# Performance work log

Hardware: AMD Instinct MI355X
Metric: run time of the kernel (lower is better)

Reference implementation:

```python
import jax, jax.numpy as jnp
import numpy as np

W0, W1 = 14, 14            # window size
NUM_HEADS = 12
DIM = 768
HEAD_DIM = DIM // NUM_HEADS
N_TOK = W0 * W1 + 1        # 197 (with cls token)
BATCH = 64


def _mask_1d_rel_pos_index(s):
    i = np.arange(s)
    return i[None, :] - i[:, None] + s - 1


def _add_cls(index, num_tokens, offset):
    index = index.reshape(num_tokens, num_tokens)
    new = np.zeros((num_tokens + 1, num_tokens + 1), dtype=np.int32)
    new[1:, 1:] = index
    new[0, :] = offset
    new[:, 0] = offset + 1
    new[0, 0] = offset + 2
    return new


def _build_rel_indices():
    nt = W0 * W1
    h = _mask_1d_rel_pos_index(W0).reshape(W0, 1, W0, 1)
    h = np.broadcast_to(h, (W0, W1, W0, W1))
    h_index = _add_cls(h, nt, 2 * W0 - 1)
    w = _mask_1d_rel_pos_index(W1).reshape(1, W1, 1, W1)
    w = np.broadcast_to(w, (W0, W1, W0, W1))
    w_index = _add_cls(w, nt, 2 * W1 - 1)
    return jnp.asarray(h_index), jnp.asarray(w_index)


def setup_inputs() -> dict:
    key = jax.random.key(0)
    ks = jax.random.split(key, 6)
    h_index, w_index = _build_rel_indices()
    return {
        "x": jax.random.normal(ks[0], (BATCH, N_TOK, DIM), dtype=jnp.float32),
        "qkv_w": jax.random.normal(ks[1], (3 * DIM, DIM), dtype=jnp.float32) * 0.02,
        "q_bias": jnp.zeros((DIM,), dtype=jnp.float32),
        "v_bias": jnp.zeros((DIM,), dtype=jnp.float32),
        "proj_w": jax.random.normal(ks[2], (DIM, DIM), dtype=jnp.float32) * 0.02,
        "proj_b": jnp.zeros((DIM,), dtype=jnp.float32),
        "rpb_high": jax.random.normal(ks[3], (2 * W0 + 2, NUM_HEADS), dtype=jnp.float32) * 0.02,
        "rpb_width": jax.random.normal(ks[4], (2 * W1 + 2, NUM_HEADS), dtype=jnp.float32) * 0.02,
        "h_index": h_index,
        "w_index": w_index,
    }


def reference(x, qkv_w, q_bias, v_bias, proj_w, proj_b, rpb_high, rpb_width,
              h_index, w_index):
    B, N, C = x.shape
    scale = HEAD_DIM ** (-0.5)
    # fused qkv with (q_bias, 0, v_bias) bias as in torch source
    bias = jnp.concatenate([q_bias, jnp.zeros_like(v_bias), v_bias])
    qkv = x @ qkv_w.T + bias                             # [B, N, 3*C]
    qkv = qkv.reshape(B, N, 3, NUM_HEADS, HEAD_DIM).transpose(2, 0, 3, 1, 4)
    q, k, v = qkv[0], qkv[1], qkv[2]                     # [B, H, N, hd]
    q = q * scale
    # qk_float=True -> scores in float32
    attn = jnp.einsum('bhnd,bhmd->bhnm',
                      q.astype(jnp.float32), k.astype(jnp.float32))
    # decoupled relative position bias: two embedding lookups, summed
    rpb = rpb_high[h_index] + rpb_width[w_index]         # [N, N, H]
    rpb = rpb.transpose(2, 0, 1)                         # [H, N, N]
    attn = attn + rpb[None].astype(attn.dtype)
    attn = jax.nn.softmax(attn, axis=-1).astype(x.dtype)
    out = jnp.einsum('bhnm,bhmd->bnhd', attn, v).reshape(B, N, C)
    return out @ proj_w.T + proj_b
```

## Files before the change

### kernel.cpp

```cpp
#include <hip/hip_runtime.h>
#include <hip/hip_bf16.h>
#include <cstdint>
#include <cstddef>

using fx4  = __attribute__((ext_vector_type(4))) float;
using bfx8 = __attribute__((ext_vector_type(8))) short;
using sx4  = __attribute__((ext_vector_type(4))) short;

#define DEV __device__ __forceinline__

static constexpr int BATCH = 64;
static constexpr int NTOK  = 197;
static constexpr int NH    = 12;
static constexpr int HD    = 64;
static constexpr int MROWS = BATCH * NTOK;
static constexpr int MPAD  = 12800;
static constexpr int KDIM  = 768;

DEV unsigned short f2bf(float f) {
  unsigned u = __builtin_bit_cast(unsigned, f);
  u += 0x7FFFu + ((u >> 16) & 1u);
  return (unsigned short)(u >> 16);
}

DEV void gload16(const unsigned short* g, unsigned short* l) {
  __builtin_amdgcn_global_load_lds(
      (const __attribute__((address_space(1))) unsigned int*)g,
      (__attribute__((address_space(3))) unsigned int*)l, 16, 0, 0);
}

DEV int xcd_swizzle(int orig, int nwg) {
  int q = nwg >> 3, r = nwg & 7;
  int xcd = orig & 7, lid = orig >> 3;
  return (xcd < r ? xcd * (q + 1) : r * (q + 1) + (xcd - r) * q) + lid;
}

__global__ void rpb_kernel(const float* __restrict__ rh, const float* __restrict__ rw,
                           const int* __restrict__ hidx, const int* __restrict__ widx,
                           float* __restrict__ rpb)
{
  int e = blockIdx.x * 256 + threadIdx.x;
  const int NN = NTOK * NTOK;
  if (e >= NH * NN) return;
  int h = e / NN, ij = e % NN;
  rpb[e] = rh[hidx[ij] * NH + h] + rw[widx[ij] * NH + h];
}

__global__ void cvt_kernel(const float* __restrict__ in,
                           unsigned short* __restrict__ out,
                           int nvec, int nvec_pad)
{
  for (int v = blockIdx.x * 256 + threadIdx.x; v < nvec_pad; v += gridDim.x * 256) {
    fx4 x = (v < nvec) ? ((const fx4*)in)[v] : fx4{0.f, 0.f, 0.f, 0.f};
    sx4 h4;
    #pragma unroll
    for (int q = 0; q < 4; q++) h4[q] = (short)f2bf(x[q]);
    ((sx4*)out)[v] = h4;
  }
}

template<int NT, int MODE>
__global__ __launch_bounds__(512, 4)
void gemm_bf16_kernel(const unsigned short* __restrict__ A,
                      const unsigned short* __restrict__ B,
                      const float* __restrict__ bias0, const float* __restrict__ bias1,
                      unsigned short* __restrict__ qb, unsigned short* __restrict__ kb,
                      unsigned short* __restrict__ vb, float* __restrict__ outp)
{
  __shared__ unsigned short At[256 * 64];
  __shared__ unsigned short Bt[128 * 64];

  const int t  = threadIdx.x;
  const int w  = t >> 6, l = t & 63;
  const int wr = w >> 1, wc = w & 1;
  const int fr = l & 15, g = l >> 4;
  const int bid = xcd_swizzle(blockIdx.x, gridDim.x);
  const int bm = bid / NT, bn = bid % NT;

  const int srow = w * 8 + (l >> 3);
  const int sgr8 = ((l & 7) ^ ((l >> 3) & 7)) * 8;

  auto STAGE = [&](int k0) {
    #pragma unroll
    for (int rd = 0; rd < 4; rd++) {
      int arow = bm * 256 + rd * 64 + srow;
      gload16(A + (size_t)arow * KDIM + k0 + sgr8, &At[(rd * 512 + w * 64) * 8]);
    }
    #pragma unroll
    for (int rd = 0; rd < 2; rd++) {
      int brow = bn * 128 + rd * 64 + srow;
      gload16(B + (size_t)brow * KDIM + k0 + sgr8, &Bt[(rd * 512 + w * 64) * 8]);
    }
  };

  fx4 acc[4][4];
  #pragma unroll
  for (int i = 0; i < 4; i++)
    #pragma unroll
    for (int j = 0; j < 4; j++) acc[i][j] = fx4{0.f, 0.f, 0.f, 0.f};

  const int a_r0 = wr * 64 + fr;
  const int b_r0 = wc * 64 + fr;
  const int swz7 = fr & 7;

  #pragma unroll 1
  for (int kt = 0; kt < 12; kt++) {
    __syncthreads();
    STAGE(kt * 64);
    __syncthreads();

    #pragma unroll
    for (int ks = 0; ks < 2; ks++) {
      const int gsw = ((ks * 4 + g) ^ swz7) * 8;
      bfx8 fb[4];
      #pragma unroll
      for (int j = 0; j < 4; j++)
        fb[j] = *(const bfx8*)&Bt[(b_r0 + j * 16) * 64 + gsw];
      #pragma unroll
      for (int i = 0; i < 4; i++) {
        bfx8 fa = *(const bfx8*)&At[(a_r0 + i * 16) * 64 + gsw];
        #pragma unroll
        for (int j = 0; j < 4; j++)
          acc[i][j] = __builtin_amdgcn_mfma_f32_16x16x32_bf16(fa, fb[j], acc[i][j], 0, 0, 0);
      }
    }
  }

  #pragma unroll
  for (int i = 0; i < 4; i++) {
    #pragma unroll
    for (int j = 0; j < 4; j++) {
      #pragma unroll
      for (int r = 0; r < 4; r++) {
        int row = bm * 256 + wr * 64 + i * 16 + g * 4 + r;
        int col = bn * 128 + wc * 64 + j * 16 + fr;
        if (row >= MROWS) continue;
        float v = acc[i][j][r];
        if (MODE == 0) {
          int which = col / 768;
          int hh = (col >> 6) % 12;
          int d  = col & 63;
          int b  = row / NTOK, n = row % NTOK;
          size_t o = (((size_t)(b * NH + hh)) * NTOK + n) * HD + d;
          if (which == 0)      qb[o] = f2bf((v + bias0[col]) * 0.125f);
          else if (which == 1) kb[o] = f2bf(v);
          else                 vb[o] = f2bf(v + bias1[col - 1536]);
        } else {
          outp[(size_t)row * 768 + col] = v + bias0[col];
        }
      }
    }
  }
}

__global__ __launch_bounds__(256)
void attn_mfma_kernel(const unsigned short* __restrict__ qf,
                      const unsigned short* __restrict__ kf,
                      const unsigned short* __restrict__ vf,
                      const float* __restrict__ rpb,
                      unsigned short* __restrict__ of)
{
  __shared__ union {
    short Kb[224 * 72];
    struct { short Pb[64 * 232]; short Vt[32 * 232]; } p;
  } u;

  const int t  = threadIdx.x;
  const int w  = t >> 6, l = t & 63;
  const int fr = l & 15, g = l >> 4;
  const int bx = xcd_swizzle(blockIdx.x, BATCH * NH * 4);
  const int b  = bx / (NH * 4);
  const int h  = (bx / 4) % NH;
  const int qt = bx & 3;
  const size_t base = ((size_t)(b * NH + h)) * NTOK * HD;
  const unsigned short* qg = qf + base;
  const unsigned short* kg = kf + base;
  const unsigned short* vg = vf + base;
  const float* rhb = rpb + (size_t)h * (NTOK * NTOK);

  const bfx8 z8 = bfx8{0,0,0,0,0,0,0,0};
  const int qrow0 = qt * 64 + w * 16 + g * 4;

  fx4 sc[14];
  #pragma unroll
  for (int j = 0; j < 14; j++) {
    int key = j * 16 + fr;
    #pragma unroll
    for (int r = 0; r < 4; r++) {
      int qrow = qrow0 + r;
      sc[j][r] = (key < NTOK && qrow < NTOK) ? rhb[qrow * NTOK + key] : 0.f;
    }
  }

  const int qrow_f = qt * 64 + w * 16 + fr;
  bfx8 aq0 = z8, aq1 = z8;
  if (qrow_f < NTOK) {
    aq0 = *(const bfx8*)(qg + (size_t)qrow_f * HD + g * 8);
    aq1 = *(const bfx8*)(qg + (size_t)qrow_f * HD + 32 + g * 8);
  }

  sx4 vreg[7];
  auto VLOAD = [&](int hf) {
    #pragma unroll
    for (int rep = 0; rep < 7; rep++) {
      int task = rep * 256 + t;
      int m  = task >> 3;
      int dq = task & 7;
      vreg[rep] = (m < NTOK)
          ? *(const sx4*)(vg + (size_t)m * HD + hf * 32 + dq * 4)
          : sx4{0, 0, 0, 0};
    }
  };
  auto VWRITE = [&]() {
    #pragma unroll
    for (int rep = 0; rep < 7; rep++) {
      int task = rep * 256 + t;
      int m  = task >> 3;
      int dq = task & 7;
      #pragma unroll
      for (int q2 = 0; q2 < 4; q2++)
        u.p.Vt[(dq * 4 + q2) * 232 + m] = vreg[rep][q2];
    }
  };

  VLOAD(0);

  {
    const int rr = t >> 3, c8 = (t & 7) * 8;
    #pragma unroll
    for (int p = 0; p < 7; p++) {
      int r = p * 32 + rr;
      bfx8 o8 = (r < NTOK) ? *(const bfx8*)(kg + (size_t)r * HD + c8) : z8;
      *(bfx8*)&u.Kb[r * 72 + c8] = o8;
    }
  }
  __syncthreads();

  #pragma unroll
  for (int j = 0; j < 14; j++) {
    bfx8 k0 = *(const bfx8*)&u.Kb[(j * 16 + fr) * 72 + g * 8];
    bfx8 k1 = *(const bfx8*)&u.Kb[(j * 16 + fr) * 72 + 32 + g * 8];
    sc[j] = __builtin_amdgcn_mfma_f32_16x16x32_bf16(aq0, k0, sc[j], 0, 0, 0);
    sc[j] = __builtin_amdgcn_mfma_f32_16x16x32_bf16(aq1, k1, sc[j], 0, 0, 0);
  }

  #pragma unroll
  for (int j = 12; j < 14; j++) {
    int key = j * 16 + fr;
    if (key >= NTOK) {
      #pragma unroll
      for (int r = 0; r < 4; r++) sc[j][r] = -1e30f;
    }
  }

  float inv4[4];
  #pragma unroll
  for (int r = 0; r < 4; r++) {
    float m = sc[0][r];
    #pragma unroll
    for (int j = 1; j < 14; j++) m = fmaxf(m, sc[j][r]);
    #pragma unroll
    for (int off = 1; off < 16; off <<= 1) m = fmaxf(m, __shfl_xor(m, off));
    float sum = 0.f;
    #pragma unroll
    for (int j = 0; j < 14; j++) {
      float e = __expf(sc[j][r] - m);
      sc[j][r] = e; sum += e;
    }
    #pragma unroll
    for (int off = 1; off < 16; off <<= 1) sum += __shfl_xor(sum, off);
    inv4[r] = 1.0f / sum;
  }

  __syncthreads();

  #pragma unroll
  for (int j = 0; j < 14; j++) {
    int key = j * 16 + fr;
    #pragma unroll
    for (int r = 0; r < 4; r++)
      u.p.Pb[(w * 16 + g * 4 + r) * 232 + key] = (short)f2bf(sc[j][r]);
  }
  VWRITE();
  __syncthreads();

  fx4 o2[4];
  #pragma unroll
  for (int j = 0; j < 4; j++) o2[j] = fx4{0.f, 0.f, 0.f, 0.f};

  VLOAD(1);

  #pragma unroll
  for (int kc = 0; kc < 7; kc++) {
    bfx8 pa = *(const bfx8*)&u.p.Pb[(w * 16 + fr) * 232 + kc * 32 + g * 8];
    #pragma unroll
    for (int jj = 0; jj < 2; jj++) {
      bfx8 vbb = *(const bfx8*)&u.p.Vt[(jj * 16 + fr) * 232 + kc * 32 + g * 8];
      o2[jj] = __builtin_amdgcn_mfma_f32_16x16x32_bf16(pa, vbb, o2[jj], 0, 0, 0);
    }
  }

  __syncthreads();
  VWRITE();
  __syncthreads();

  #pragma unroll
  for (int kc = 0; kc < 7; kc++) {
    bfx8 pa = *(const bfx8*)&u.p.Pb[(w * 16 + fr) * 232 + kc * 32 + g * 8];
    #pragma unroll
    for (int jj = 0; jj < 2; jj++) {
      bfx8 vbb = *(const bfx8*)&u.p.Vt[(jj * 16 + fr) * 232 + kc * 32 + g * 8];
      o2[2 + jj] = __builtin_amdgcn_mfma_f32_16x16x32_bf16(pa, vbb, o2[2 + jj], 0, 0, 0);
    }
  }

  #pragma unroll
  for (int r = 0; r < 4; r++) {
    int qrow = qt * 64 + w * 16 + g * 4 + r;
    if (qrow < NTOK) {
      float inv = inv4[r];
      #pragma unroll
      for (int j = 0; j < 4; j++)
        of[((size_t)(b * NTOK + qrow)) * 768 + h * 64 + j * 16 + fr]
            = f2bf(o2[j][r] * inv);
    }
  }
}

extern "C" void kernel_launch(void* const* d_in, const int* in_sizes, int n_in,
                              void* d_out, int out_size, void* d_ws, size_t ws_size,
                              hipStream_t stream)
{
  const float* x      = (const float*)d_in[0];
  const float* qkv_w  = (const float*)d_in[1];
  const float* q_bias = (const float*)d_in[2];
  const float* v_bias = (const float*)d_in[3];
  const float* proj_w = (const float*)d_in[4];
  const float* proj_b = (const float*)d_in[5];
  const float* rpb_h  = (const float*)d_in[6];
  const float* rpb_w  = (const float*)d_in[7];
  const int*   h_idx  = (const int*)d_in[8];
  const int*   w_idx  = (const int*)d_in[9];
  float* out = (float*)d_out;

  char* ws = (char*)d_ws;
  size_t off = 0;
  auto alloc = [&](size_t bytes) { size_t o = off; off += (bytes + 255) & ~(size_t)255; return o; };

  const size_t QKV_ELEMS = (size_t)BATCH * NH * NTOK * HD;
  unsigned short* Axb = (unsigned short*)(ws + alloc((size_t)MPAD * KDIM * 2));
  unsigned short* Bqb = (unsigned short*)(ws + alloc((size_t)2304 * KDIM * 2));
  unsigned short* Bpb = (unsigned short*)(ws + alloc((size_t)768 * KDIM * 2));
  unsigned short* qb  = (unsigned short*)(ws + alloc(QKV_ELEMS * 2));
  unsigned short* kb  = (unsigned short*)(ws + alloc(QKV_ELEMS * 2));
  unsigned short* vb  = (unsigned short*)(ws + alloc(QKV_ELEMS * 2));
  float*          rpb = (float*)(ws + alloc((size_t)NH * NTOK * NTOK * 4));
  unsigned short* ofb = (unsigned short*)(ws + alloc((size_t)MPAD * KDIM * 2));
  (void)ws_size; (void)in_sizes; (void)n_in; (void)out_size;

  const int nvec_x  = MROWS * KDIM / 4;
  const int nvec_xp = MPAD * KDIM / 4;

  cvt_kernel<<<2048, 256, 0, stream>>>(x, Axb, nvec_x, nvec_xp);
  cvt_kernel<<<1024, 256, 0, stream>>>(qkv_w, Bqb, 2304 * KDIM / 4, 2304 * KDIM / 4);
  cvt_kernel<<<512, 256, 0, stream>>>(proj_w, Bpb, 768 * KDIM / 4, 768 * KDIM / 4);
  {
    int total = NH * NTOK * NTOK;
    rpb_kernel<<<(total + 255) / 256, 256, 0, stream>>>(rpb_h, rpb_w, h_idx, w_idx, rpb);
  }
  hipMemsetAsync(ofb + (size_t)MROWS * KDIM, 0,
                 (size_t)(MPAD - MROWS) * KDIM * 2, stream);
  gemm_bf16_kernel<18, 0><<<50 * 18, 512, 0, stream>>>(
      Axb, Bqb, q_bias, v_bias, qb, kb, vb, nullptr);
  attn_mfma_kernel<<<BATCH * NH * 4, 256, 0, stream>>>(qb, kb, vb, rpb, ofb);
  gemm_bf16_kernel<6, 1><<<50 * 6, 512, 0, stream>>>(
      ofb, Bpb, proj_b, nullptr, nullptr, nullptr, nullptr, out);
}
```

Measured before the change: 177.1 us.

## Double-buffer GEMM LDS tiles with async prefetch and use 128x128 tiles

The bf16 GEMM moves from 256x128 tiles with 512 threads and a single LDS buffer to 128x128 tiles with 256 threads and two LDS buffers. Global-to-LDS loads for tile k+2 are issued while tile k is being computed, with vmcnt waits and raw barriers in place of the two full syncthreads per iteration. This is meant to hide global load latency and give more blocks, improving load balance across CUs. In exchange, each block does less reuse per loaded byte, and correctness now depends on the hand-set vmcnt values.

```diff
diff --git a/kernel.cpp b/kernel.cpp
--- a/kernel.cpp
+++ b/kernel.cpp
@@ -60,15 +60,15 @@
 }
 
 template<int NT, int MODE>
-__global__ __launch_bounds__(512, 4)
+__global__ __launch_bounds__(256, 2)
 void gemm_bf16_kernel(const unsigned short* __restrict__ A,
                       const unsigned short* __restrict__ B,
                       const float* __restrict__ bias0, const float* __restrict__ bias1,
                       unsigned short* __restrict__ qb, unsigned short* __restrict__ kb,
                       unsigned short* __restrict__ vb, float* __restrict__ outp)
 {
-  __shared__ unsigned short At[256 * 64];
-  __shared__ unsigned short Bt[128 * 64];
+  __shared__ unsigned short At[2][128 * 64];
+  __shared__ unsigned short Bt[2][128 * 64];
 
   const int t  = threadIdx.x;
   const int w  = t >> 6, l = t & 63;
@@ -80,16 +80,17 @@
   const int srow = w * 8 + (l >> 3);
   const int sgr8 = ((l & 7) ^ ((l >> 3) & 7)) * 8;
 
-  auto STAGE = [&](int k0) {
+  auto STAGE = [&](int kt, int c) {
+    const int k0 = kt * 64;
     #pragma unroll
     for (int rd = 0; rd < 4; rd++) {
-      int arow = bm * 256 + rd * 64 + srow;
-      gload16(A + (size_t)arow * KDIM + k0 + sgr8, &At[(rd * 512 + w * 64) * 8]);
-    }
-    #pragma unroll
-    for (int rd = 0; rd < 2; rd++) {
-      int brow = bn * 128 + rd * 64 + srow;
-      gload16(B + (size_t)brow * KDIM + k0 + sgr8, &Bt[(rd * 512 + w * 64) * 8]);
+      int arow = bm * 128 + rd * 32 + srow;
+      gload16(A + (size_t)arow * KDIM + k0 + sgr8, &At[c][(rd * 256 + w * 64) * 8]);
+    }
+    #pragma unroll
+    for (int rd = 0; rd < 4; rd++) {
+      int brow = bn * 128 + rd * 32 + srow;
+      gload16(B + (size_t)brow * KDIM + k0 + sgr8, &Bt[c][(rd * 256 + w * 64) * 8]);
     }
   };
 
@@ -103,11 +104,16 @@
   const int b_r0 = wc * 64 + fr;
   const int swz7 = fr & 7;
 
+  STAGE(0, 0);
+  STAGE(1, 1);
+
   #pragma unroll 1
   for (int kt = 0; kt < 12; kt++) {
-    __syncthreads();
-    STAGE(kt * 64);
-    __syncthreads();
+    const int c = kt & 1;
+    if (kt < 11) asm volatile("s_waitcnt vmcnt(8)" ::: "memory");
+    else         asm volatile("s_waitcnt vmcnt(0)" ::: "memory");
+    __builtin_amdgcn_s_barrier();
+    asm volatile("" ::: "memory");
 
     #pragma unroll
     for (int ks = 0; ks < 2; ks++) {
@@ -115,15 +121,21 @@
       bfx8 fb[4];
       #pragma unroll
       for (int j = 0; j < 4; j++)
-        fb[j] = *(const bfx8*)&Bt[(b_r0 + j * 16) * 64 + gsw];
+        fb[j] = *(const bfx8*)&Bt[c][(b_r0 + j * 16) * 64 + gsw];
       #pragma unroll
       for (int i = 0; i < 4; i++) {
-        bfx8 fa = *(const bfx8*)&At[(a_r0 + i * 16) * 64 + gsw];
+        bfx8 fa = *(const bfx8*)&At[c][(a_r0 + i * 16) * 64 + gsw];
         #pragma unroll
         for (int j = 0; j < 4; j++)
           acc[i][j] = __builtin_amdgcn_mfma_f32_16x16x32_bf16(fa, fb[j], acc[i][j], 0, 0, 0);
       }
     }
+
+    asm volatile("s_waitcnt lgkmcnt(0)" ::: "memory");
+    __builtin_amdgcn_sched_barrier(0);
+    __builtin_amdgcn_s_barrier();
+    asm volatile("" ::: "memory");
+    if (kt + 2 < 12) STAGE(kt + 2, c);
   }
 
   #pragma unroll
@@ -132,7 +144,7 @@
     for (int j = 0; j < 4; j++) {
       #pragma unroll
       for (int r = 0; r < 4; r++) {
-        int row = bm * 256 + wr * 64 + i * 16 + g * 4 + r;
+        int row = bm * 128 + wr * 64 + i * 16 + g * 4 + r;
         int col = bn * 128 + wc * 64 + j * 16 + fr;
         if (row >= MROWS) continue;
         float v = acc[i][j][r];
@@ -370,9 +382,9 @@
   }
   hipMemsetAsync(ofb + (size_t)MROWS * KDIM, 0,
                  (size_t)(MPAD - MROWS) * KDIM * 2, stream);
-  gemm_bf16_kernel<18, 0><<<50 * 18, 512, 0, stream>>>(
+  gemm_bf16_kernel<18, 0><<<99 * 18, 256, 0, stream>>>(
       Axb, Bqb, q_bias, v_bias, qb, kb, vb, nullptr);
   attn_mfma_kernel<<<BATCH * NH * 4, 256, 0, stream>>>(qb, kb, vb, rpb, ofb);
-  gemm_bf16_kernel<6, 1><<<50 * 6, 512, 0, stream>>>(
+  gemm_bf16_kernel<6, 1><<<99 * 6, 256, 0, stream>>>(
       ofb, Bpb, proj_b, nullptr, nullptr, nullptr, nullptr, out);
 }
```

Result: slower. 220.1 us (+24.3%).
